# Kernel tuning notes

Measured on AMD Instinct MI355X. Metric: run time of the kernel, lower is better.

Reference implementation:

```python
import jax, jax.numpy as jnp
import numpy as np
from jax import lax

B_, L_, C_IN = 32, 1024, 3
D_MODEL, D_STATE, D_CONV, EXPAND = 256, 16, 4, 2
D_INNER = EXPAND * D_MODEL           # 512
DT_RANK = D_MODEL // 16              # 16
N_HEADS, N_CLASS = 8, 10
LN_EPS = 1e-5


def _pos_emb(L, d):
    pos = np.arange(L, dtype=np.float32)[:, None]
    div = np.exp(np.arange(0, d, 2, dtype=np.float32) * (-np.log(10000.0) / d))
    pe = np.zeros((L, d), np.float32)
    pe[:, 0::2] = np.sin(pos * div)
    pe[:, 1::2] = np.cos(pos * div)
    return jnp.asarray(pe)


def setup_inputs() -> dict:
    key = jax.random.key(0)
    ks = jax.random.split(key, 12)
    f = lambda k, shp, s: jax.random.normal(k, shp, jnp.float32) * s
    return {
        'x_enc': f(ks[0], (B_, L_, C_IN), 1.0),
        'x_mark_enc': jnp.ones((B_, L_), jnp.float32),
        'conv_emb_w': f(ks[1], (D_MODEL, C_IN, 3), (2.0 / (C_IN * 3)) ** 0.5),
        'in_proj_w': f(ks[2], (2 * D_INNER, D_MODEL), D_MODEL ** -0.5),
        'conv1d_w': f(ks[3], (D_INNER, 1, D_CONV), D_CONV ** -0.5),
        'conv1d_b': f(ks[4], (D_INNER,), 0.02),
        'x_proj_w': f(ks[5], (DT_RANK + 2 * D_STATE, D_INNER), D_INNER ** -0.5),
        'dt_proj_w': f(ks[6], (D_INNER, DT_RANK), DT_RANK ** -0.5),
        'dt_proj_b': f(ks[7], (D_INNER,), 0.1) - 2.0,
        'A_log': jnp.log(jnp.tile(jnp.arange(1, D_STATE + 1, dtype=jnp.float32), (D_INNER, 1))),
        'D': jnp.ones((D_INNER,), jnp.float32),
        'out_proj_w': f(ks[8], (D_MODEL, D_INNER), D_INNER ** -0.5),
        'ln_g': jnp.ones((D_MODEL,), jnp.float32),
        'ln_b': jnp.zeros((D_MODEL,), jnp.float32),
        'out_w': f(ks[9], (N_CLASS, D_MODEL), D_MODEL ** -0.5),
        'attn_w': f(ks[10], (N_HEADS, D_MODEL), 0.02),
        'attn_b': jnp.ones((N_HEADS,), jnp.float32),
    }


def _forward(x_enc, x_mark_enc, conv_emb_w, in_proj_w, conv1d_w, conv1d_b,
             x_proj_w, dt_proj_w, dt_proj_b, A_log, D, out_proj_w,
             ln_g, ln_b, out_w, attn_w, attn_b):
    silu = jax.nn.silu
    # --- embedding: Conv1d 'same' with replicate padding + sinusoidal PE ---
    xp = jnp.pad(x_enc, ((0, 0), (1, 1), (0, 0)), mode='edge')      # k=3 -> pad (1,1)
    x = lax.conv_general_dilated(xp.transpose(0, 2, 1), conv_emb_w, (1,), 'VALID',
                                 dimension_numbers=('NCH', 'OIH', 'NCH')).transpose(0, 2, 1)
    x = x + _pos_emb(L_, D_MODEL)[None]                              # (B,L,D)

    # --- Mamba_TimeVariant (standard Mamba selective scan) ---
    xz = jnp.einsum('bld,ed->ble', x, in_proj_w)                     # (B,L,2*Din)
    xin, z = xz[..., :D_INNER], xz[..., D_INNER:]
    # depthwise causal conv, kernel D_CONV
    xc = jnp.pad(xin.transpose(0, 2, 1), ((0, 0), (0, 0), (D_CONV - 1, 0)))
    xc = lax.conv_general_dilated(xc, conv1d_w, (1,), 'VALID',
                                  feature_group_count=D_INNER,
                                  dimension_numbers=('NCH', 'OIH', 'NCH'))
    xc = silu(xc.transpose(0, 2, 1) + conv1d_b)                      # (B,L,Din)

    dbl = jnp.einsum('bld,ed->ble', xc, x_proj_w)                    # (B,L,dt_rank+2*N)
    dtr = dbl[..., :DT_RANK]
    Bm = dbl[..., DT_RANK:DT_RANK + D_STATE]                         # (B,L,N)
    Cm = dbl[..., DT_RANK + D_STATE:]                                # (B,L,N)
    dt = jax.nn.softplus(jnp.einsum('blr,dr->bld', dtr, dt_proj_w) + dt_proj_b)
    A = -jnp.exp(A_log)                                              # (Din,N)

    def step(h, inp):
        dt_t, B_t, C_t, x_t = inp                                    # (B,Din),(B,N),(B,N),(B,Din)
        dA = jnp.exp(dt_t[..., None] * A)                            # (B,Din,N)
        h = dA * h + dt_t[..., None] * B_t[:, None, :] * x_t[..., None]
        y = jnp.einsum('bdn,bn->bd', h, C_t)
        return h, y

    h0 = jnp.zeros((B_, D_INNER, D_STATE), xc.dtype)
    inputs = (dt.transpose(1, 0, 2), Bm.transpose(1, 0, 2),
              Cm.transpose(1, 0, 2), xc.transpose(1, 0, 2))
    _, ys = lax.scan(step, h0, inputs)                               # (L,B,Din)
    y = ys.transpose(1, 0, 2) + xc * D                               # skip via D
    y = y * silu(z)
    m = jnp.einsum('bld,ed->ble', y, out_proj_w)                     # (B,L,Dmodel)

    # LayerNorm + SiLU
    mu = m.mean(-1, keepdims=True)
    var = ((m - mu) ** 2).mean(-1, keepdims=True)
    m = (m - mu) * lax.rsqrt(var + LN_EPS) * ln_g + ln_b
    m = silu(m)

    # classification head
    logit = jnp.einsum('bld,cd->blc', m, out_w) * x_mark_enc[..., None]
    s = jnp.einsum('bld,hd->blh', m, attn_w) + attn_b                # (B,L,H)
    w = jax.nn.softmax(jnp.max(s, axis=2, keepdims=True), axis=1)    # (B,L,1)
    return (logit * w).sum(1)                                        # (B,num_class)


def reference(x_enc, x_mark_enc, conv_emb_w, in_proj_w, conv1d_w, conv1d_b,
              x_proj_w, dt_proj_w, dt_proj_b, A_log, D, out_proj_w,
              ln_g, ln_b, out_w, attn_w, attn_b):
    return _forward(x_enc, x_mark_enc, conv_emb_w, in_proj_w, conv1d_w, conv1d_b,
                    x_proj_w, dt_proj_w, dt_proj_b, A_log, D, out_proj_w,
                    ln_g, ln_b, out_w, attn_w, attn_b)
```

## Files before the change

### kernel.cpp

```cpp
#include <hip/hip_runtime.h>
#include <hip/hip_bf16.h>
#include <math.h>

#define B_  32
#define L_  1024
#define CIN 3
#define DM  256
#define DI  512
#define NST 16
#define NH  8
#define NC  10
#define M_TOT (B_*L_)

typedef unsigned short u16;
typedef __attribute__((ext_vector_type(8))) short bf16x8;
typedef __attribute__((ext_vector_type(4))) float f32x4;

static __device__ __forceinline__ float sigmoidf_(float x) {
    return 1.0f / (1.0f + __expf(-x));
}
static __device__ __forceinline__ u16 f2bf(float f) {
    unsigned int u = __float_as_uint(f);
    return (u16)((u + 0x7FFF + ((u >> 16) & 1)) >> 16);
}
static __device__ __forceinline__ float bf2f(u16 u) {
    return __uint_as_float(((unsigned int)u) << 16);
}

static __device__ __forceinline__ void reduce8_pair(float& a, float& b) {
    asm volatile(
        "s_nop 1\n\t"
        "v_add_f32 %0, %0, %0 quad_perm:[1,0,3,2] row_mask:0xf bank_mask:0xf\n\t"
        "v_add_f32 %1, %1, %1 quad_perm:[1,0,3,2] row_mask:0xf bank_mask:0xf\n\t"
        "s_nop 1\n\t"
        "v_add_f32 %0, %0, %0 quad_perm:[2,3,0,1] row_mask:0xf bank_mask:0xf\n\t"
        "v_add_f32 %1, %1, %1 quad_perm:[2,3,0,1] row_mask:0xf bank_mask:0xf\n\t"
        "s_nop 1\n\t"
        "v_add_f32 %0, %0, %0 row_half_mirror row_mask:0xf bank_mask:0xf\n\t"
        "v_add_f32 %1, %1, %1 row_half_mirror row_mask:0xf bank_mask:0xf\n\t"
        "s_nop 1\n\t"
        : "+v"(a), "+v"(b));
}

__global__ __launch_bounds__(256) void k_cvt(const float* __restrict__ in,
        u16* __restrict__ out) {
    int i = (blockIdx.x * 256 + threadIdx.x) * 4;
    float4 v = *(const float4*)(in + i);
    ushort4 o;
    o.x = f2bf(v.x); o.y = f2bf(v.y); o.z = f2bf(v.z); o.w = f2bf(v.w);
    *(ushort4*)(out + i) = o;
}

__global__ __launch_bounds__(256) void k_embed(const float* __restrict__ xe,
        const float* __restrict__ w, u16* __restrict__ x) {
    int bl = blockIdx.x;
    int l = bl & (L_-1);
    int b = bl >> 10;
    int d = threadIdx.x;
    const float* xb = xe + (size_t)b * L_ * CIN;
    int t0 = l > 0 ? l-1 : 0;
    int t2 = l < L_-1 ? l+1 : L_-1;
    const float* w3 = w + d*9;
    float acc = 0.f;
    #pragma unroll
    for (int i = 0; i < 3; ++i) {
        acc += xb[t0*3+i] * w3[i*3+0];
        acc += xb[l *3+i] * w3[i*3+1];
        acc += xb[t2*3+i] * w3[i*3+2];
    }
    int j = d >> 1;
    float div = expf((float)(2*j) * (-logf(10000.0f)/(float)DM));
    float ang = (float)l * div;
    acc += (d & 1) ? cosf(ang) : sinf(ang);
    x[(size_t)bl*DM + d] = f2bf(acc);
}

#define GST 40
__global__ __launch_bounds__(256) void k_gemm_mfma(
        const u16* __restrict__ A, const u16* __restrict__ W,
        float* __restrict__ O1f, u16* __restrict__ O1b,
        u16* __restrict__ O2b, int M, int N, int K, int S) {
    __shared__ u16 As[128*GST];
    __shared__ u16 Bs[128*GST];
    int tid = threadIdx.x;
    int row0 = blockIdx.y * 128, col0 = blockIdx.x * 128;
    int wave = tid >> 6, lane = tid & 63;
    int wr = (wave >> 1) * 64, wc = (wave & 1) * 64;
    int l16 = lane & 15, kl = lane >> 4;
    int srow = tid >> 1, skh = (tid & 1) * 16;
    const u16* Ag = A + (size_t)(row0 + srow) * K + skh;
    const u16* Wg = W + (size_t)(col0 + srow) * K + skh;

    f32x4 acc[4][4];
    #pragma unroll
    for (int m = 0; m < 4; ++m)
        #pragma unroll
        for (int n = 0; n < 4; ++n)
            acc[m][n] = (f32x4){0.f, 0.f, 0.f, 0.f};

    for (int k0 = 0; k0 < K; k0 += 32) {
        uint4 a0 = *(const uint4*)(Ag + k0);
        uint4 a1 = *(const uint4*)(Ag + k0 + 8);
        uint4 b0 = *(const uint4*)(Wg + k0);
        uint4 b1 = *(const uint4*)(Wg + k0 + 8);
        __syncthreads();
        *(uint4*)&As[srow*GST + skh]     = a0;
        *(uint4*)&As[srow*GST + skh + 8] = a1;
        *(uint4*)&Bs[srow*GST + skh]     = b0;
        *(uint4*)&Bs[srow*GST + skh + 8] = b1;
        __syncthreads();
        bf16x8 af[4], bf[4];
        #pragma unroll
        for (int m = 0; m < 4; ++m)
            af[m] = *(const bf16x8*)&As[(wr + m*16 + l16)*GST + kl*8];
        #pragma unroll
        for (int n = 0; n < 4; ++n)
            bf[n] = *(const bf16x8*)&Bs[(wc + n*16 + l16)*GST + kl*8];
        #pragma unroll
        for (int m = 0; m < 4; ++m)
            #pragma unroll
            for (int n = 0; n < 4; ++n)
                acc[m][n] = __builtin_amdgcn_mfma_f32_16x16x32_bf16(
                                af[m], bf[n], acc[m][n], 0, 0, 0);
    }

    #pragma unroll
    for (int m = 0; m < 4; ++m) {
        int rbase = row0 + wr + m*16 + kl*4;
        #pragma unroll
        for (int n = 0; n < 4; ++n) {
            int col = col0 + wc + n*16 + l16;
            #pragma unroll
            for (int r = 0; r < 4; ++r) {
                float v = acc[m][n][r];
                if (col < S) {
                    if (O1b) O1b[(size_t)(rbase + r)*S + col] = f2bf(v);
                    else     O1f[(size_t)(rbase + r)*S + col] = v;
                } else {
                    O2b[(size_t)(rbase + r)*(N - S) + (col - S)] = f2bf(v);
                }
            }
        }
    }
}

__global__ __launch_bounds__(256) void k_conv(const u16* __restrict__ xin,
        const float* __restrict__ w, const float* __restrict__ bias,
        u16* __restrict__ xc) {
    size_t i4 = (size_t)blockIdx.x * 256 + threadIdx.x;
    int d4 = (int)(i4 & (DI/4 - 1)) * 4;
    size_t m = i4 >> 7;
    int l = (int)(m & (L_-1));
    float4 wv0 = *(const float4*)(w + (size_t)(d4+0)*4);
    float4 wv1 = *(const float4*)(w + (size_t)(d4+1)*4);
    float4 wv2 = *(const float4*)(w + (size_t)(d4+2)*4);
    float4 wv3 = *(const float4*)(w + (size_t)(d4+3)*4);
    float W[4][4] = {{wv0.x,wv0.y,wv0.z,wv0.w},{wv1.x,wv1.y,wv1.z,wv1.w},
                     {wv2.x,wv2.y,wv2.z,wv2.w},{wv3.x,wv3.y,wv3.z,wv3.w}};
    float4 acc = *(const float4*)(bias + d4);
    #pragma unroll
    for (int k = 0; k < 4; ++k) {
        int t = l + k - 3;
        if (t >= 0) {
            ushort4 xv = *(const ushort4*)(xin + (m + k - 3)*DI + d4);
            acc.x = fmaf(bf2f(xv.x), W[0][k], acc.x);
            acc.y = fmaf(bf2f(xv.y), W[1][k], acc.y);
            acc.z = fmaf(bf2f(xv.z), W[2][k], acc.z);
            acc.w = fmaf(bf2f(xv.w), W[3][k], acc.w);
        }
    }
    ushort4 r;
    r.x = f2bf(acc.x * sigmoidf_(acc.x));
    r.y = f2bf(acc.y * sigmoidf_(acc.y));
    r.z = f2bf(acc.z * sigmoidf_(acc.z));
    r.w = f2bf(acc.w * sigmoidf_(acc.w));
    *(ushort4*)(xc + m*DI + d4) = r;
}

#define XBM 128
#define XBK 16
__global__ __launch_bounds__(256) void k_xproj(const u16* __restrict__ xc,
        const float* __restrict__ wp, float* __restrict__ dbl) {
    __shared__ float As[XBK][XBM];
    __shared__ float Ws[XBK][48];
    int tid = threadIdx.x;
    int row0 = blockIdx.x * XBM;
    int lr = tid >> 1;
    int lk = (tid & 1) * 8;
    int we = tid >> 2;
    int wk = (tid & 3) * 4;
    int tx = tid & 15;
    int ty = tid >> 4;
    float acc[8][3];
    #pragma unroll
    for (int i = 0; i < 8; ++i)
        #pragma unroll
        for (int j = 0; j < 3; ++j) acc[i][j] = 0.f;

    for (int k0 = 0; k0 < DI; k0 += XBK) {
        ushort4 ab0 = *(const ushort4*)(xc + (size_t)(row0+lr)*DI + k0 + lk);
        ushort4 ab1 = *(const ushort4*)(xc + (size_t)(row0+lr)*DI + k0 + lk + 4);
        float4 w0 = make_float4(0.f,0.f,0.f,0.f);
        if (tid < 192) w0 = *(const float4*)(wp + (size_t)we*DI + k0 + wk);
        __syncthreads();
        As[lk+0][lr]=bf2f(ab0.x); As[lk+1][lr]=bf2f(ab0.y);
        As[lk+2][lr]=bf2f(ab0.z); As[lk+3][lr]=bf2f(ab0.w);
        As[lk+4][lr]=bf2f(ab1.x); As[lk+5][lr]=bf2f(ab1.y);
        As[lk+6][lr]=bf2f(ab1.z); As[lk+7][lr]=bf2f(ab1.w);
        if (tid < 192) {
            Ws[wk+0][we]=w0.x; Ws[wk+1][we]=w0.y; Ws[wk+2][we]=w0.z; Ws[wk+3][we]=w0.w;
        }
        __syncthreads();
        #pragma unroll
        for (int k = 0; k < XBK; ++k) {
            float4 av0 = *(const float4*)&As[k][ty*8];
            float4 av1 = *(const float4*)&As[k][ty*8+4];
            float w0_ = Ws[k][tx*3+0];
            float w1_ = Ws[k][tx*3+1];
            float w2_ = Ws[k][tx*3+2];
            float ar[8] = {av0.x,av0.y,av0.z,av0.w,av1.x,av1.y,av1.z,av1.w};
            #pragma unroll
            for (int i = 0; i < 8; ++i) {
                acc[i][0] = fmaf(ar[i], w0_, acc[i][0]);
                acc[i][1] = fmaf(ar[i], w1_, acc[i][1]);
                acc[i][2] = fmaf(ar[i], w2_, acc[i][2]);
            }
        }
    }
    #pragma unroll
    for (int i = 0; i < 8; ++i) {
        size_t r = row0 + ty*8 + i;
        #pragma unroll
        for (int j = 0; j < 3; ++j)
            dbl[r*48 + tx*3 + j] = acc[i][j];
    }
}

__global__ __launch_bounds__(256) void k_dtproj(const float* __restrict__ dbl,
        const float* __restrict__ dtw, const float* __restrict__ dtb,
        float* __restrict__ dt) {
    __shared__ float wl[DI][17];
    __shared__ float rl[32][16];
    size_t m0 = (size_t)blockIdx.x * 32;
    for (int i = threadIdx.x; i < DI*16; i += 256)
        wl[i >> 4][i & 15] = dtw[i];
    for (int i = threadIdx.x; i < 32*16; i += 256)
        rl[i >> 4][i & 15] = dbl[(m0 + (i>>4))*48 + (i & 15)];
    __syncthreads();
    float b0 = dtb[threadIdx.x];
    float b1 = dtb[256 + threadIdx.x];
    for (int mm = 0; mm < 32; ++mm) {
        #pragma unroll
        for (int half = 0; half < 2; ++half) {
            int d = half*256 + threadIdx.x;
            float acc = half ? b1 : b0;
            #pragma unroll
            for (int r = 0; r < 16; ++r)
                acc = fmaf(rl[mm][r], wl[d][r], acc);
            float sp = fmaxf(acc, 0.f) + log1pf(__expf(-fabsf(acc)));
            dt[(m0+mm)*DI + d] = sp;
        }
    }
}

#define SCAN_T 64
__global__ __launch_bounds__(256) void k_scan(const float* __restrict__ dt,
        const u16* __restrict__ xcb, const float* __restrict__ dbl,
        const float* __restrict__ A_log, const float* __restrict__ Dp,
        const u16* __restrict__ zbf, u16* __restrict__ ybf) {
    __shared__ float4 sq4[SCAN_T*33];
    __shared__ float2 sBC2[SCAN_T*18];

    int tid = threadIdx.x;
    int wave = tid >> 6, lane = tid & 63;
    int chw = lane >> 3;
    int j   = lane & 7;
    int ch  = wave*8 + chw;
    int d0 = blockIdx.x * 32;
    int b  = blockIdx.y;
    int d  = d0 + ch;
    float Aa = -expf(A_log[(size_t)d*NST + 2*j])     * 1.44269504f;
    float Ab = -expf(A_log[(size_t)d*NST + 2*j + 1]) * 1.44269504f;
    float h0 = 0.f, h1 = 0.f;
    size_t base = (size_t)b * L_;

    int st = tid >> 2;
    int sc = (tid & 3) * 8;
    int ns = (tid & 3) * 4;
    float4 Dva = *(const float4*)(Dp + d0 + sc);
    float4 Dvb = *(const float4*)(Dp + d0 + sc + 4);

    for (int t0 = 0; t0 < L_; t0 += SCAN_T) {
        __syncthreads();
        {
            size_t row = base + t0 + st;
            float4 dtv0 = *(const float4*)(dt + row*DI + d0 + sc);
            float4 dtv1 = *(const float4*)(dt + row*DI + d0 + sc + 4);
            uint4 xv = *(const uint4*)(xcb + row*DI + d0 + sc);
            uint4 zv = *(const uint4*)(zbf + row*DI + d0 + sc);
            float4 Bv = *(const float4*)(dbl + row*48 + 16 + ns);
            float4 Cv = *(const float4*)(dbl + row*48 + 32 + ns);
            float xr[8] = { bf2f((u16)(xv.x & 0xffff)), bf2f((u16)(xv.x >> 16)),
                            bf2f((u16)(xv.y & 0xffff)), bf2f((u16)(xv.y >> 16)),
                            bf2f((u16)(xv.z & 0xffff)), bf2f((u16)(xv.z >> 16)),
                            bf2f((u16)(xv.w & 0xffff)), bf2f((u16)(xv.w >> 16)) };
            float zr[8] = { bf2f((u16)(zv.x & 0xffff)), bf2f((u16)(zv.x >> 16)),
                            bf2f((u16)(zv.y & 0xffff)), bf2f((u16)(zv.y >> 16)),
                            bf2f((u16)(zv.z & 0xffff)), bf2f((u16)(zv.z >> 16)),
                            bf2f((u16)(zv.w & 0xffff)), bf2f((u16)(zv.w >> 16)) };
            float dtr[8] = { dtv0.x, dtv0.y, dtv0.z, dtv0.w,
                             dtv1.x, dtv1.y, dtv1.z, dtv1.w };
            float Dr[8] = { Dva.x, Dva.y, Dva.z, Dva.w,
                            Dvb.x, Dvb.y, Dvb.z, Dvb.w };
            #pragma unroll
            for (int k = 0; k < 8; ++k) {
                float g = zr[k] * sigmoidf_(zr[k]);
                sq4[st*33 + sc + k] = make_float4(dtr[k], dtr[k]*xr[k],
                                                  xr[k]*Dr[k]*g, g);
            }
            *(float4*)&sBC2[st*18 + ns]     = make_float4(Bv.x, Cv.x, Bv.y, Cv.y);
            *(float4*)&sBC2[st*18 + ns + 2] = make_float4(Bv.z, Cv.z, Bv.w, Cv.w);
        }
        __syncthreads();

        #pragma unroll 2
        for (int t2 = 0; t2 < SCAN_T/2; ++t2) {
            float4 bc0 = *(const float4*)&sBC2[(2*t2)*18 + 2*j];
            float4 bc1 = *(const float4*)&sBC2[(2*t2+1)*18 + 2*j];
            float4 q0 = sq4[(2*t2)*33 + ch];
            float4 q1 = sq4[(2*t2+1)*33 + ch];
            float dA0 = exp2f(q0.x * Aa);
            float dA1 = exp2f(q0.x * Ab);
            h0 = fmaf(dA0, h0, q0.y * bc0.x);
            h1 = fmaf(dA1, h1, q0.y * bc0.z);
            float p0 = fmaf(h1, bc0.w, h0 * bc0.y);
            dA0 = exp2f(q1.x * Aa);
            dA1 = exp2f(q1.x * Ab);
            h0 = fmaf(dA0, h0, q1.y * bc1.x);
            h1 = fmaf(dA1, h1, q1.y * bc1.z);
            float p1 = fmaf(h1, bc1.w, h0 * bc1.y);
            reduce8_pair(p0, p1);
            if (j == 0) {
                size_t row = base + t0 + 2*t2;
                ybf[row*DI + d]     = f2bf(fmaf(p0, q0.w, q0.z));
                ybf[(row+1)*DI + d] = f2bf(fmaf(p1, q1.w, q1.z));
            }
        }
    }
}

__global__ __launch_bounds__(256) void k_lnsilu(float* __restrict__ m,
        const float* __restrict__ g, const float* __restrict__ bta) {
    size_t row = (size_t)blockIdx.x*4 + (threadIdx.x >> 6);
    int lane = threadIdx.x & 63;
    float4 v = *(const float4*)(m + row*DM + lane*4);
    float s = v.x + v.y + v.z + v.w;
    #pragma unroll
    for (int o = 32; o > 0; o >>= 1) s += __shfl_xor(s, o);
    float mu = s * (1.0f/DM);
    float4 c = make_float4(v.x-mu, v.y-mu, v.z-mu, v.w-mu);
    float s2 = c.x*c.x + c.y*c.y + c.z*c.z + c.w*c.w;
    #pragma unroll
    for (int o = 32; o > 0; o >>= 1) s2 += __shfl_xor(s2, o);
    float rstd = 1.0f / sqrtf(s2 * (1.0f/DM) + 1e-5f);
    float4 gv = *(const float4*)(g + lane*4);
    float4 bv = *(const float4*)(bta + lane*4);
    float o0 = c.x*rstd*gv.x + bv.x;
    float o1 = c.y*rstd*gv.y + bv.y;
    float o2 = c.z*rstd*gv.z + bv.z;
    float o3 = c.w*rstd*gv.w + bv.w;
    float4 r;
    r.x = o0 * sigmoidf_(o0);
    r.y = o1 * sigmoidf_(o1);
    r.z = o2 * sigmoidf_(o2);
    r.w = o3 * sigmoidf_(o3);
    *(float4*)(m + row*DM + lane*4) = r;
}

#define HBK 32
__global__ __launch_bounds__(256) void k_heads18(const float* __restrict__ m,
        const float* __restrict__ aw, const float* __restrict__ ow,
        float* __restrict__ r18) {
    __shared__ float As[128][36];
    __shared__ float Ws[18][36];
    int tid = threadIdx.x;
    int row0 = blockIdx.x * 128;
    int r = tid >> 1, ch = tid & 1, cb = ch * 9;
    int sr = tid >> 1, sk = (tid & 1) * 16;
    float acc[9];
    #pragma unroll
    for (int c = 0; c < 9; ++c) acc[c] = 0.f;

    for (int k0 = 0; k0 < DM; k0 += HBK) {
        float4 a[4];
        #pragma unroll
        for (int q = 0; q < 4; ++q)
            a[q] = *(const float4*)(m + (size_t)(row0+sr)*DM + k0 + sk + q*4);
        float4 wv = make_float4(0.f,0.f,0.f,0.f);
        int wc = tid >> 3, wk = (tid & 7) * 4;
        if (tid < 144) {
            const float* wsrc = (wc < NH) ? (aw + wc*DM) : (ow + (wc-NH)*DM);
            wv = *(const float4*)(wsrc + k0 + wk);
        }
        __syncthreads();
        #pragma unroll
        for (int q = 0; q < 4; ++q)
            *(float4*)&As[sr][sk + q*4] = a[q];
        if (tid < 144)
            *(float4*)&Ws[wc][wk] = wv;
        __syncthreads();
        #pragma unroll
        for (int k4 = 0; k4 < HBK/4; ++k4) {
            float4 av = *(const float4*)&As[r][k4*4];
            #pragma unroll
            for (int c = 0; c < 9; ++c) {
                float4 w4 = *(const float4*)&Ws[cb + c][k4*4];
                acc[c] += av.x*w4.x + av.y*w4.y + av.z*w4.z + av.w*w4.w;
            }
        }
        __syncthreads();
    }
    #pragma unroll
    for (int c = 0; c < 9; ++c)
        r18[(size_t)(row0 + r)*18 + cb + c] = acc[c];
}

__global__ __launch_bounds__(256) void k_final(const float* __restrict__ r18,
        const float* __restrict__ ab, const float* __restrict__ xmark,
        float* __restrict__ out) {
    __shared__ float e[L_];
    __shared__ float red[256];
    int b = blockIdx.x;
    int tid = threadIdx.x;
    float abr[NH];
    #pragma unroll
    for (int j = 0; j < NH; ++j) abr[j] = ab[j];
    float mx = -1e30f;
    for (int l = tid; l < L_; l += 256) {
        const float* rr = r18 + ((size_t)b*L_ + l)*18;
        float sm = rr[0] + abr[0];
        #pragma unroll
        for (int j = 1; j < NH; ++j) sm = fmaxf(sm, rr[j] + abr[j]);
        e[l] = sm;
        mx = fmaxf(mx, sm);
    }
    #pragma unroll
    for (int o = 32; o > 0; o >>= 1) mx = fmaxf(mx, __shfl_xor(mx, o));
    red[tid] = mx;
    __syncthreads();
    mx = fmaxf(fmaxf(red[0], red[64]), fmaxf(red[128], red[192]));
    __syncthreads();
    float ssum = 0.f;
    for (int l = tid; l < L_; l += 256) {
        float ev = __expf(e[l] - mx);
        e[l] = ev;
        ssum += ev;
    }
    #pragma unroll
    for (int o = 32; o > 0; o >>= 1) ssum += __shfl_xor(ssum, o);
    if ((tid & 63) == 0) red[tid >> 6] = ssum;
    __syncthreads();
    float inv = 1.0f / (red[0]+red[1]+red[2]+red[3]);
    float acc[NC];
    #pragma unroll
    for (int c = 0; c < NC; ++c) acc[c] = 0.f;
    for (int l = tid; l < L_; l += 256) {
        float wl = e[l] * xmark[(size_t)b*L_ + l];
        const float* lg = r18 + ((size_t)b*L_ + l)*18 + NH;
        #pragma unroll
        for (int c = 0; c < NC; ++c) acc[c] = fmaf(wl, lg[c], acc[c]);
    }
    __syncthreads();
    for (int c = 0; c < NC; ++c) {
        red[tid] = acc[c];
        __syncthreads();
        if (tid < 64) {
            float s2 = red[tid]+red[tid+64]+red[tid+128]+red[tid+192];
            #pragma unroll
            for (int o = 32; o > 0; o >>= 1) s2 += __shfl_xor(s2, o);
            if (tid == 0) out[(size_t)b*NC + c] = s2 * inv;
        }
        __syncthreads();
    }
}

extern "C" void kernel_launch(void* const* d_in, const int* in_sizes, int n_in,
                              void* d_out, int out_size, void* d_ws, size_t ws_size,
                              hipStream_t stream) {
    const float* x_enc  = (const float*)d_in[0];
    const float* x_mark = (const float*)d_in[1];
    const float* cemb_w = (const float*)d_in[2];
    const float* inp_w  = (const float*)d_in[3];
    const float* c1_w   = (const float*)d_in[4];
    const float* c1_b   = (const float*)d_in[5];
    const float* xp_w   = (const float*)d_in[6];
    const float* dtp_w  = (const float*)d_in[7];
    const float* dtp_b  = (const float*)d_in[8];
    const float* A_log  = (const float*)d_in[9];
    const float* Dp     = (const float*)d_in[10];
    const float* outp_w = (const float*)d_in[11];
    const float* ln_g   = (const float*)d_in[12];
    const float* ln_b   = (const float*)d_in[13];
    const float* out_w  = (const float*)d_in[14];
    const float* attn_w = (const float*)d_in[15];
    const float* attn_b = (const float*)d_in[16];
    float* out = (float*)d_out;

    char* ws = (char*)d_ws;
    size_t o = 0;
    u16*   xbf  = (u16*)(ws + o);   o += (size_t)M_TOT*DM*2;
    u16*   xinb = (u16*)(ws + o);   o += (size_t)M_TOT*DI*2;
    u16*   zbf  = (u16*)(ws + o);   o += (size_t)M_TOT*DI*2;
    u16*   xcb  = (u16*)(ws + o);   o += (size_t)M_TOT*DI*2;
    u16*   ybf  = (u16*)(ws + o);   o += (size_t)M_TOT*DI*2;
    float* dt   = (float*)(ws + o); o += (size_t)M_TOT*DI*4;
    float* mm   = (float*)(ws + o); o += (size_t)M_TOT*DM*4;
    float* dbl  = (float*)(ws + o); o += (size_t)M_TOT*48*4;
    u16*   wbfi = (u16*)(ws + o);   o += (size_t)2*DI*DM*2;
    u16*   wbfo = (u16*)(ws + o);   o += (size_t)DM*DI*2;
    float* r18  = (float*)(ws + o); o += (size_t)M_TOT*18*4;

    k_cvt   <<<(2*DI*DM)/1024, 256, 0, stream>>>(inp_w, wbfi);
    k_cvt   <<<(DM*DI)/1024, 256, 0, stream>>>(outp_w, wbfo);
    k_embed <<<M_TOT, 256, 0, stream>>>(x_enc, cemb_w, xbf);
    k_gemm_mfma<<<dim3(8, M_TOT/128), 256, 0, stream>>>(xbf, wbfi,
                                nullptr, xinb, zbf, M_TOT, 2*DI, DM, DI);
    k_conv  <<<(M_TOT*DI/4)/256, 256, 0, stream>>>(xinb, c1_w, c1_b, xcb);
    k_xproj <<<M_TOT/XBM, 256, 0, stream>>>(xcb, xp_w, dbl);
    k_dtproj<<<M_TOT/32, 256, 0, stream>>>(dbl, dtp_w, dtp_b, dt);
    k_scan  <<<dim3(DI/32, B_), 256, 0, stream>>>(dt, xcb, dbl, A_log, Dp,
                                                  zbf, ybf);
    k_gemm_mfma<<<dim3(2, M_TOT/128), 256, 0, stream>>>(ybf, wbfo,
                                mm, nullptr, zbf, M_TOT, DM, DI, DM);
    k_lnsilu<<<M_TOT/4, 256, 0, stream>>>(mm, ln_g, ln_b);
    k_heads18<<<M_TOT/128, 256, 0, stream>>>(mm, attn_w, out_w, r18);
    k_final <<<B_, 256, 0, stream>>>(r18, attn_b, x_mark, out);
}
```

Before: 463.3 us.

## Store dt and out-proj output in bf16, fuse LayerNorm+SiLU into heads kernel

The dt intermediate is now written and read as bf16 instead of fp32, halving scan input traffic for that tensor. The out-projection GEMM writes bf16 through its bf16 output path, and the separate LayerNorm+SiLU kernel is removed. The heads kernel now computes row mean and variance itself in one pass, then normalises and applies SiLU while staging into shared memory. This removes a full read/write pass over m and one kernel launch, at the cost of extra bf16 rounding on dt and m. Variance now uses the E[x^2]-mu^2 form, and the trailing barrier in the heads loop was dropped, which may introduce a shared-memory race on As/Ws between iterations.

```diff
diff --git a/kernel.cpp b/kernel.cpp
--- a/kernel.cpp
+++ b/kernel.cpp
@@ -25,6 +25,9 @@
 }
 static __device__ __forceinline__ float bf2f(u16 u) {
     return __uint_as_float(((unsigned int)u) << 16);
+}
+static __device__ __forceinline__ float2 bf2x2(unsigned int u) {
+    return make_float2(bf2f((u16)(u & 0xffff)), bf2f((u16)(u >> 16)));
 }
 
 static __device__ __forceinline__ void reduce8_pair(float& a, float& b) {
@@ -238,7 +241,7 @@
 
 __global__ __launch_bounds__(256) void k_dtproj(const float* __restrict__ dbl,
         const float* __restrict__ dtw, const float* __restrict__ dtb,
-        float* __restrict__ dt) {
+        u16* __restrict__ dt) {
     __shared__ float wl[DI][17];
     __shared__ float rl[32][16];
     size_t m0 = (size_t)blockIdx.x * 32;
@@ -258,13 +261,13 @@
             for (int r = 0; r < 16; ++r)
                 acc = fmaf(rl[mm][r], wl[d][r], acc);
             float sp = fmaxf(acc, 0.f) + log1pf(__expf(-fabsf(acc)));
-            dt[(m0+mm)*DI + d] = sp;
+            dt[(m0+mm)*DI + d] = f2bf(sp);
         }
     }
 }
 
 #define SCAN_T 64
-__global__ __launch_bounds__(256) void k_scan(const float* __restrict__ dt,
+__global__ __launch_bounds__(256) void k_scan(const u16* __restrict__ dt,
         const u16* __restrict__ xcb, const float* __restrict__ dbl,
         const float* __restrict__ A_log, const float* __restrict__ Dp,
         const u16* __restrict__ zbf, u16* __restrict__ ybf) {
@@ -294,22 +297,23 @@
         __syncthreads();
         {
             size_t row = base + t0 + st;
-            float4 dtv0 = *(const float4*)(dt + row*DI + d0 + sc);
-            float4 dtv1 = *(const float4*)(dt + row*DI + d0 + sc + 4);
+            uint4 dv = *(const uint4*)(dt  + row*DI + d0 + sc);
             uint4 xv = *(const uint4*)(xcb + row*DI + d0 + sc);
             uint4 zv = *(const uint4*)(zbf + row*DI + d0 + sc);
             float4 Bv = *(const float4*)(dbl + row*48 + 16 + ns);
             float4 Cv = *(const float4*)(dbl + row*48 + 32 + ns);
-            float xr[8] = { bf2f((u16)(xv.x & 0xffff)), bf2f((u16)(xv.x >> 16)),
-                            bf2f((u16)(xv.y & 0xffff)), bf2f((u16)(xv.y >> 16)),
-                            bf2f((u16)(xv.z & 0xffff)), bf2f((u16)(xv.z >> 16)),
-                            bf2f((u16)(xv.w & 0xffff)), bf2f((u16)(xv.w >> 16)) };
-            float zr[8] = { bf2f((u16)(zv.x & 0xffff)), bf2f((u16)(zv.x >> 16)),
-                            bf2f((u16)(zv.y & 0xffff)), bf2f((u16)(zv.y >> 16)),
-                            bf2f((u16)(zv.z & 0xffff)), bf2f((u16)(zv.z >> 16)),
-                            bf2f((u16)(zv.w & 0xffff)), bf2f((u16)(zv.w >> 16)) };
-            float dtr[8] = { dtv0.x, dtv0.y, dtv0.z, dtv0.w,
-                             dtv1.x, dtv1.y, dtv1.z, dtv1.w };
+            float2 dt01 = bf2x2(dv.x), dt23 = bf2x2(dv.y);
+            float2 dt45 = bf2x2(dv.z), dt67 = bf2x2(dv.w);
+            float2 x01 = bf2x2(xv.x), x23 = bf2x2(xv.y);
+            float2 x45 = bf2x2(xv.z), x67 = bf2x2(xv.w);
+            float2 z01 = bf2x2(zv.x), z23 = bf2x2(zv.y);
+            float2 z45 = bf2x2(zv.z), z67 = bf2x2(zv.w);
+            float dtr[8] = { dt01.x, dt01.y, dt23.x, dt23.y,
+                             dt45.x, dt45.y, dt67.x, dt67.y };
+            float xr[8]  = { x01.x, x01.y, x23.x, x23.y,
+                             x45.x, x45.y, x67.x, x67.y };
+            float zr[8]  = { z01.x, z01.y, z23.x, z23.y,
+                             z45.x, z45.y, z67.x, z67.y };
             float Dr[8] = { Dva.x, Dva.y, Dva.z, Dva.w,
                             Dvb.x, Dvb.y, Dvb.z, Dvb.w };
             #pragma unroll
@@ -349,53 +353,47 @@
     }
 }
 
-__global__ __launch_bounds__(256) void k_lnsilu(float* __restrict__ m,
-        const float* __restrict__ g, const float* __restrict__ bta) {
-    size_t row = (size_t)blockIdx.x*4 + (threadIdx.x >> 6);
-    int lane = threadIdx.x & 63;
-    float4 v = *(const float4*)(m + row*DM + lane*4);
-    float s = v.x + v.y + v.z + v.w;
-    #pragma unroll
-    for (int o = 32; o > 0; o >>= 1) s += __shfl_xor(s, o);
-    float mu = s * (1.0f/DM);
-    float4 c = make_float4(v.x-mu, v.y-mu, v.z-mu, v.w-mu);
-    float s2 = c.x*c.x + c.y*c.y + c.z*c.z + c.w*c.w;
-    #pragma unroll
-    for (int o = 32; o > 0; o >>= 1) s2 += __shfl_xor(s2, o);
-    float rstd = 1.0f / sqrtf(s2 * (1.0f/DM) + 1e-5f);
-    float4 gv = *(const float4*)(g + lane*4);
-    float4 bv = *(const float4*)(bta + lane*4);
-    float o0 = c.x*rstd*gv.x + bv.x;
-    float o1 = c.y*rstd*gv.y + bv.y;
-    float o2 = c.z*rstd*gv.z + bv.z;
-    float o3 = c.w*rstd*gv.w + bv.w;
-    float4 r;
-    r.x = o0 * sigmoidf_(o0);
-    r.y = o1 * sigmoidf_(o1);
-    r.z = o2 * sigmoidf_(o2);
-    r.w = o3 * sigmoidf_(o3);
-    *(float4*)(m + row*DM + lane*4) = r;
-}
-
 #define HBK 32
-__global__ __launch_bounds__(256) void k_heads18(const float* __restrict__ m,
+__global__ __launch_bounds__(256) void k_lnheads18(const u16* __restrict__ mb,
+        const float* __restrict__ g, const float* __restrict__ bta,
         const float* __restrict__ aw, const float* __restrict__ ow,
         float* __restrict__ r18) {
     __shared__ float As[128][36];
     __shared__ float Ws[18][36];
+    __shared__ float gb[DM], bb[DM];
     int tid = threadIdx.x;
     int row0 = blockIdx.x * 128;
-    int r = tid >> 1, ch = tid & 1, cb = ch * 9;
     int sr = tid >> 1, sk = (tid & 1) * 16;
+    gb[tid] = g[tid];
+    bb[tid] = bta[tid];
+    const u16* mrow = mb + (size_t)(row0 + sr)*DM;
+
+    float s1 = 0.f, s2 = 0.f;
+    for (int k0 = 0; k0 < DM; k0 += HBK) {
+        uint4 va = *(const uint4*)(mrow + k0 + sk);
+        uint4 vb = *(const uint4*)(mrow + k0 + sk + 8);
+        unsigned int ua[8] = {va.x, va.y, va.z, va.w, vb.x, vb.y, vb.z, vb.w};
+        #pragma unroll
+        for (int q = 0; q < 8; ++q) {
+            float2 p = bf2x2(ua[q]);
+            s1 += p.x + p.y;
+            s2 += p.x*p.x + p.y*p.y;
+        }
+    }
+    s1 += __shfl_xor(s1, 1);
+    s2 += __shfl_xor(s2, 1);
+    float mu = s1 * (1.0f/DM);
+    float var = fmaxf(s2 * (1.0f/DM) - mu*mu, 0.f);
+    float rstd = 1.0f / sqrtf(var + 1e-5f);
+
+    int r = tid >> 1, cb = (tid & 1) * 9;
     float acc[9];
     #pragma unroll
     for (int c = 0; c < 9; ++c) acc[c] = 0.f;
 
     for (int k0 = 0; k0 < DM; k0 += HBK) {
-        float4 a[4];
-        #pragma unroll
-        for (int q = 0; q < 4; ++q)
-            a[q] = *(const float4*)(m + (size_t)(row0+sr)*DM + k0 + sk + q*4);
+        uint4 va = *(const uint4*)(mrow + k0 + sk);
+        uint4 vb = *(const uint4*)(mrow + k0 + sk + 8);
         float4 wv = make_float4(0.f,0.f,0.f,0.f);
         int wc = tid >> 3, wk = (tid & 7) * 4;
         if (tid < 144) {
@@ -403,11 +401,20 @@
             wv = *(const float4*)(wsrc + k0 + wk);
         }
         __syncthreads();
-        #pragma unroll
-        for (int q = 0; q < 4; ++q)
-            *(float4*)&As[sr][sk + q*4] = a[q];
-        if (tid < 144)
-            *(float4*)&Ws[wc][wk] = wv;
+        {
+            unsigned int ua[8] = {va.x, va.y, va.z, va.w, vb.x, vb.y, vb.z, vb.w};
+            #pragma unroll
+            for (int q = 0; q < 8; ++q) {
+                float2 p = bf2x2(ua[q]);
+                int c0 = k0 + sk + 2*q;
+                float o0 = (p.x - mu)*rstd*gb[c0]   + bb[c0];
+                float o1 = (p.y - mu)*rstd*gb[c0+1] + bb[c0+1];
+                As[sr][sk + 2*q]     = o0 * sigmoidf_(o0);
+                As[sr][sk + 2*q + 1] = o1 * sigmoidf_(o1);
+            }
+            if (tid < 144)
+                *(float4*)&Ws[wc][wk] = wv;
+        }
         __syncthreads();
         #pragma unroll
         for (int k4 = 0; k4 < HBK/4; ++k4) {
@@ -418,7 +425,6 @@
                 acc[c] += av.x*w4.x + av.y*w4.y + av.z*w4.z + av.w*w4.w;
             }
         }
-        __syncthreads();
     }
     #pragma unroll
     for (int c = 0; c < 9; ++c)
@@ -513,8 +519,8 @@
     u16*   zbf  = (u16*)(ws + o);   o += (size_t)M_TOT*DI*2;
     u16*   xcb  = (u16*)(ws + o);   o += (size_t)M_TOT*DI*2;
     u16*   ybf  = (u16*)(ws + o);   o += (size_t)M_TOT*DI*2;
-    float* dt   = (float*)(ws + o); o += (size_t)M_TOT*DI*4;
-    float* mm   = (float*)(ws + o); o += (size_t)M_TOT*DM*4;
+    u16*   dt16 = (u16*)(ws + o);   o += (size_t)M_TOT*DI*2;
+    u16*   mm16 = (u16*)(ws + o);   o += (size_t)M_TOT*DM*2;
     float* dbl  = (float*)(ws + o); o += (size_t)M_TOT*48*4;
     u16*   wbfi = (u16*)(ws + o);   o += (size_t)2*DI*DM*2;
     u16*   wbfo = (u16*)(ws + o);   o += (size_t)DM*DI*2;
@@ -527,12 +533,12 @@
                                 nullptr, xinb, zbf, M_TOT, 2*DI, DM, DI);
     k_conv  <<<(M_TOT*DI/4)/256, 256, 0, stream>>>(xinb, c1_w, c1_b, xcb);
     k_xproj <<<M_TOT/XBM, 256, 0, stream>>>(xcb, xp_w, dbl);
-    k_dtproj<<<M_TOT/32, 256, 0, stream>>>(dbl, dtp_w, dtp_b, dt);
-    k_scan  <<<dim3(DI/32, B_), 256, 0, stream>>>(dt, xcb, dbl, A_log, Dp,
+    k_dtproj<<<M_TOT/32, 256, 0, stream>>>(dbl, dtp_w, dtp_b, dt16);
+    k_scan  <<<dim3(DI/32, B_), 256, 0, stream>>>(dt16, xcb, dbl, A_log, Dp,
                                                   zbf, ybf);
     k_gemm_mfma<<<dim3(2, M_TOT/128), 256, 0, stream>>>(ybf, wbfo,
-                                mm, nullptr, zbf, M_TOT, DM, DI, DM);
-    k_lnsilu<<<M_TOT/4, 256, 0, stream>>>(mm, ln_g, ln_b);
-    k_heads18<<<M_TOT/128, 256, 0, stream>>>(mm, attn_w, out_w, r18);
+                                nullptr, mm16, zbf, M_TOT, DM, DI, DM);
+    k_lnheads18<<<M_TOT/128, 256, 0, stream>>>(mm16, ln_g, ln_b, attn_w,
+                                               out_w, r18);
     k_final <<<B_, 256, 0, stream>>>(r18, attn_b, x_mark, out);
 }
```

After: 440.7 us. 4.9% less time.
